# Kernel tuning notes

Measured on AMD Instinct MI355X. Metric: run time of the kernel, lower is better.

Reference implementation:

```python
import jax, jax.numpy as jnp
import numpy as np

N = 16384      # nodes
E = 262144     # edges (avg degree 16)
T = 4          # type_num
D = 64         # d_model
L = 2          # layers


def setup_inputs() -> dict:
    key = jax.random.key(0)
    ks = jax.random.split(key, 7)
    return {
        "x": jax.random.normal(ks[0], (N, D), dtype=jnp.float32),
        "edge_feature": jax.random.normal(ks[1], (T, D), dtype=jnp.float32),
        "theta": jax.random.normal(ks[2], (L, T, 3 * D), dtype=jnp.float32) * (1.0 / np.sqrt(3 * D)),
        "wr": jax.random.normal(ks[3], (L, D, D), dtype=jnp.float32) * (1.0 / np.sqrt(D)),
        "we": jax.random.normal(ks[4], (L, D, D), dtype=jnp.float32) * (1.0 / np.sqrt(D)),
        "edge_index": jax.random.randint(ks[5], (2, E), 0, N, dtype=jnp.int64),
        "edge_type": jax.random.randint(ks[6], (E,), 0, T, dtype=jnp.int64),
    }


def _scatter_softmax(r, row, num_nodes):
    # r: [T, E]; softmax over edges grouped by destination node `row`.
    rT = r.T  # [E, T] (segment ops reduce over leading axis)
    m = jax.ops.segment_max(rT, row, num_segments=num_nodes)   # [N, T]
    e = jnp.exp(rT - m[row])                                    # [E, T]
    s = jax.ops.segment_sum(e, row, num_segments=num_nodes)     # [N, T]
    return (e / s[row]).T                                       # [T, E]


def reference(x, edge_feature, theta, wr, we, edge_index, edge_type):
    n, d = x.shape
    t = edge_feature.shape[0]
    num_layers = theta.shape[0]
    row, col = edge_index[0], edge_index[1]

    h = jnp.broadcast_to(x[None], (t, n, d))  # x.expand(type_num, N, d)
    ef = edge_feature                          # [T, D]
    for i in range(num_layers):
        tg, thi, thj = theta[i, :, :d], theta[i, :, d:2 * d], theta[i, :, 2 * d:]
        # per-edge scores
        r_g = (tg @ ef.T)[:, edge_type]                        # [T, E]
        r_hi = jnp.einsum('tnd,td->tn', h, thi)[:, row]        # [T, E]
        r_hj = jnp.einsum('tnd,td->tn', h, thj)[:, col]        # [T, E]
        r = _scatter_softmax(r_g + r_hi + r_hj, row, n)        # [T, E]
        # gated messages
        ef = ef @ wr[i]                                        # [T, D]
        v_g = jax.nn.sigmoid(ef)[edge_type]                    # [E, D]
        v_h = jnp.einsum('tnd,de->tne', h, we[i])[:, col]      # [T, E, D]
        msg = r[:, :, None] * v_g[None] * v_h                  # [T, E, D]
        agg = jax.ops.segment_sum(jnp.moveaxis(msg, 1, 0), row, num_segments=n)  # [N, T, D]
        h = jnp.moveaxis(agg, 0, 1)                            # [T, N, D]
        if i < num_layers - 1:
            h = jax.nn.relu(h)      # dropout is identity in eval mode
            ef = jax.nn.relu(ef)
    return h
```

## Files before the change

kernel.cpp:

```cpp
#include <hip/hip_runtime.h>

#define NN 16384
#define EE 262144
#define TT 4
#define DD 64
#define SLOT 96
#define HB (EE / 256)
#define NB (NN / 64)

__device__ inline float g16_max(float v) {
    #pragma unroll
    for (int off = 1; off <= 8; off <<= 1) v = fmaxf(v, __shfl_xor(v, off));
    return v;
}
__device__ inline float g16_sum(float v) {
    #pragma unroll
    for (int off = 1; off <= 8; off <<= 1) v += __shfl_xor(v, off);
    return v;
}
__device__ inline float4 edge_group_reduce(float4 v) {
    #pragma unroll
    for (int off = 16; off < 64; off <<= 1) {
        v.x += __shfl_xor(v.x, off); v.y += __shfl_xor(v.y, off);
        v.z += __shfl_xor(v.z, off); v.w += __shfl_xor(v.w, off);
    }
    return v;
}
__device__ inline unsigned short f2bf(float f) {
    unsigned u = __float_as_uint(f);
    u += 0x7FFFu + ((u >> 16) & 1u);
    return (unsigned short)(u >> 16);
}
__device__ inline float bf2f(unsigned short h) {
    return __uint_as_float(((unsigned)h) << 16);
}
__device__ inline float4 bf4_to_f4(ushort4 h) {
    return float4{bf2f(h.x), bf2f(h.y), bf2f(h.z), bf2f(h.w)};
}

__global__ __launch_bounds__(256) void build_node0_kernel(
        const int* __restrict__ row, const int* __restrict__ col,
        const int* __restrict__ et, int* __restrict__ cnt,
        int* __restrict__ ce_slot,
        const float* __restrict__ x, const float* __restrict__ theta,
        const float* __restrict__ we, const float* __restrict__ ef_in,
        const float* __restrict__ wr,
        float* __restrict__ a, float* __restrict__ b,
        unsigned short* __restrict__ hw0,
        float* __restrict__ sg, float* __restrict__ rg) {
    __shared__ float h_lds[64][68];
    __shared__ float4 we_lds[64][16];
    __shared__ float th_lds[4][2][64];
    __shared__ float part_a[64][4][4];
    __shared__ float part_b[64][4][4];
    __shared__ float ef0[TT * DD];
    __shared__ float ef1[TT * DD];
    int tid = threadIdx.x;
    int bid = blockIdx.x;

    if (bid < HB) {
        int e = bid * 256 + tid;
        int r = row[e];
        int pos = atomicAdd(&cnt[r], 1);
        if (pos < SLOT)
            ce_slot[r * SLOT + pos] = col[e] | (et[e] << 14);
        return;
    }
    bid -= HB;

    if (bid == NB) {
        int t = tid >> 6, d = tid & 63;
        ef0[tid] = ef_in[tid];
        __syncthreads();
        if (tid < 16) {
            int tt = tid & 3, tq = tid >> 2;
            float s = 0.f;
            for (int k = 0; k < DD; ++k) s += theta[tq * 192 + k] * ef0[tt * DD + k];
            rg[tq * 4 + tt] = s;
        }
        float acc = 0.f;
        for (int k = 0; k < DD; ++k) acc += ef0[t * DD + k] * wr[k * DD + d];
        sg[tid] = 1.f / (1.f + __expf(-acc));
        ef1[tid] = fmaxf(acc, 0.f);
        __syncthreads();
        if (tid < 16) {
            int tt = tid & 3, tq = tid >> 2;
            float s = 0.f;
            for (int k = 0; k < DD; ++k) s += theta[(TT + tq) * 192 + k] * ef1[tt * DD + k];
            rg[16 + tq * 4 + tt] = s;
        }
        float acc2 = 0.f;
        for (int k = 0; k < DD; ++k) acc2 += ef1[t * DD + k] * wr[DD * DD + k * DD + d];
        sg[TT * DD + tid] = 1.f / (1.f + __expf(-acc2));
        return;
    }

    int n0 = bid * 64;
    {
        int q = tid & 15, nr = tid >> 4;
        #pragma unroll
        for (int r = 0; r < 4; ++r) {
            int n = r * 16 + nr;
            *(float4*)&h_lds[n][4 * q] = ((const float4*)x)[(n0 + n) * 16 + q];
        }
    }
    {
        const float4* we4 = (const float4*)we;
        #pragma unroll
        for (int r = 0; r < 4; ++r)
            ((float4*)we_lds)[tid + 256 * r] = we4[tid + 256 * r];
    }
    {
        #pragma unroll
        for (int r = 0; r < 2; ++r) {
            int e = tid + 256 * r;
            int t = e >> 7, ab = (e >> 6) & 1, k = e & 63;
            th_lds[t][ab][k] = theta[t * 192 + 64 + ab * 64 + k];
        }
    }
    __syncthreads();
    int i = tid >> 4, j = tid & 15;
    float4 acc[4];
    acc[0] = acc[1] = acc[2] = acc[3] = float4{0.f, 0.f, 0.f, 0.f};
    for (int k = 0; k < 64; ++k) {
        float4 wv = we_lds[k][j];
        #pragma unroll
        for (int r = 0; r < 4; ++r) {
            float hv = h_lds[4 * i + r][k];
            acc[r].x += hv * wv.x; acc[r].y += hv * wv.y;
            acc[r].z += hv * wv.z; acc[r].w += hv * wv.w;
        }
    }
    {
        int t = j >> 2, kq = j & 3;
        float pa[4] = {0, 0, 0, 0}, pb[4] = {0, 0, 0, 0};
        for (int kk = 0; kk < 16; ++kk) {
            int k = kq * 16 + kk;
            float ti = th_lds[t][0][k], tj = th_lds[t][1][k];
            #pragma unroll
            for (int r = 0; r < 4; ++r) {
                float hv = h_lds[4 * i + r][k];
                pa[r] += hv * ti; pb[r] += hv * tj;
            }
        }
        #pragma unroll
        for (int r = 0; r < 4; ++r) {
            part_a[4 * i + r][t][kq] = pa[r];
            part_b[4 * i + r][t][kq] = pb[r];
        }
    }
    #pragma unroll
    for (int r = 0; r < 4; ++r) {
        ushort4 hv;
        hv.x = f2bf(acc[r].x); hv.y = f2bf(acc[r].y);
        hv.z = f2bf(acc[r].z); hv.w = f2bf(acc[r].w);
        ((ushort4*)hw0)[(n0 + 4 * i + r) * 16 + j] = hv;
    }
    __syncthreads();
    {
        int n = tid >> 2, t = tid & 3;
        float4 va = *(float4*)&part_a[n][t][0];
        float4 vb = *(float4*)&part_b[n][t][0];
        a[t * NN + n0 + n] = va.x + va.y + va.z + va.w;
        b[t * NN + n0 + n] = vb.x + vb.y + vb.z + vb.w;
    }
}

__global__ __launch_bounds__(256) void node1_kernel(
        const float* __restrict__ h1, const float* __restrict__ theta,
        const float* __restrict__ we,
        float* __restrict__ a, float* __restrict__ b,
        unsigned short* __restrict__ hw) {
    __shared__ float h_lds[64][68];
    __shared__ float4 we_lds[64][16];
    __shared__ float th_lds[2][64];
    __shared__ float part_a[64][17];
    __shared__ float part_b[64][17];
    int tid = threadIdx.x;
    int t = blockIdx.y;
    int n0 = blockIdx.x * 64;
    const float* ht = h1 + (size_t)t * NN * DD;
    {
        int q = tid & 15, nr = tid >> 4;
        #pragma unroll
        for (int r = 0; r < 4; ++r) {
            int n = r * 16 + nr;
            *(float4*)&h_lds[n][4 * q] = ((const float4*)ht)[(n0 + n) * 16 + q];
        }
    }
    {
        const float4* we4 = (const float4*)(we + DD * DD);
        #pragma unroll
        for (int r = 0; r < 4; ++r)
            ((float4*)we_lds)[tid + 256 * r] = we4[tid + 256 * r];
    }
    if (tid < 128) {
        int ab = tid >> 6, k = tid & 63;
        th_lds[ab][k] = theta[(TT + t) * 192 + 64 + ab * 64 + k];
    }
    __syncthreads();
    int i = tid >> 4, j = tid & 15;
    float4 acc[4];
    acc[0] = acc[1] = acc[2] = acc[3] = float4{0.f, 0.f, 0.f, 0.f};
    for (int k = 0; k < 64; ++k) {
        float4 wv = we_lds[k][j];
        #pragma unroll
        for (int r = 0; r < 4; ++r) {
            float hv = h_lds[4 * i + r][k];
            acc[r].x += hv * wv.x; acc[r].y += hv * wv.y;
            acc[r].z += hv * wv.z; acc[r].w += hv * wv.w;
        }
    }
    {
        float pa[4] = {0, 0, 0, 0}, pb[4] = {0, 0, 0, 0};
        #pragma unroll
        for (int kk = 0; kk < 4; ++kk) {
            int k = 4 * j + kk;
            float ti = th_lds[0][k], tj = th_lds[1][k];
            #pragma unroll
            for (int r = 0; r < 4; ++r) {
                float hv = h_lds[4 * i + r][k];
                pa[r] += hv * ti; pb[r] += hv * tj;
            }
        }
        #pragma unroll
        for (int r = 0; r < 4; ++r) {
            part_a[4 * i + r][j] = pa[r];
            part_b[4 * i + r][j] = pb[r];
        }
    }
    #pragma unroll
    for (int r = 0; r < 4; ++r) {
        ushort4 hv;
        hv.x = f2bf(acc[r].x); hv.y = f2bf(acc[r].y);
        hv.z = f2bf(acc[r].z); hv.w = f2bf(acc[r].w);
        ((ushort4*)hw)[((size_t)t * NN + n0 + 4 * i + r) * 16 + j] = hv;
    }
    __syncthreads();
    if (tid < 64) {
        float s = 0.f;
        #pragma unroll
        for (int jj = 0; jj < 16; ++jj) s += part_a[tid][jj];
        a[t * NN + n0 + tid] = s;
    } else if (tid < 128) {
        int n = tid - 64;
        float s = 0.f;
        #pragma unroll
        for (int jj = 0; jj < 16; ++jj) s += part_b[n][jj];
        b[t * NN + n0 + n] = s;
    }
}

__global__ __launch_bounds__(256) void edge_agg0_kernel(
        const int* __restrict__ cnt, const int* __restrict__ ce_slot,
        const float* __restrict__ a, const float* __restrict__ b,
        const float* __restrict__ rg, const float* __restrict__ sg,
        const unsigned short* __restrict__ hw0, float* __restrict__ h1) {
    __shared__ float4 sg4[TT * 16];
    __shared__ float rg_lds[16];
    __shared__ int cols[4][SLOT];
    __shared__ float wT[4][SLOT][4];
    int tid = threadIdx.x;
    if (tid < 64) sg4[tid] = ((const float4*)sg)[tid];
    if (tid < 16) rg_lds[tid] = rg[tid];
    int w = tid >> 6, lane = tid & 63;
    int n = blockIdx.x * 4 + w;
    int deg = cnt[n];
    if (deg > SLOT) deg = SLOT;
    const int* ces = ce_slot + n * SLOT;
    int tl = lane >> 4, il = lane & 15;
    __syncthreads();

    float a_n = a[tl * NN + n];
    const float* bt = b + tl * NN;
    float m_l = -INFINITY, s_l = 0.f;
    for (int e = il; e < deg; e += 16) {
        int pk = ces[e];
        int c = pk & 16383, tt = pk >> 14;
        float rp = a_n + bt[c] + rg_lds[tl * 4 + tt];
        wT[w][e][tl] = rp;
        if (tl == 0) cols[w][e] = pk;
        if (rp > m_l) { s_l = s_l * __expf(m_l - rp) + 1.f; m_l = rp; }
        else          { s_l += __expf(rp - m_l); }
    }
    float m = g16_max(m_l);
    float s = g16_sum((m_l > -INFINITY) ? s_l * __expf(m_l - m) : 0.f);
    float inv_s = (s > 0.f) ? 1.f / s : 0.f;
    for (int e = il; e < deg; e += 16)
        wT[w][e][tl] = __expf(wT[w][e][tl] - m) * inv_s;
    __syncthreads();

    int eg = lane >> 4, q = lane & 15;
    float4 acc0{0,0,0,0}, acc1{0,0,0,0}, acc2{0,0,0,0}, acc3{0,0,0,0};
    const ushort4* hw4 = (const ushort4*)hw0;
    for (int base = 0; base < deg; base += 4) {
        int e = base + eg;
        if (e < deg) {
            int pk = cols[w][e];
            int c = pk & 16383, tt = pk >> 14;
            ushort4 hv = hw4[c * 16 + q];
            float4 sgv = sg4[tt * 16 + q];
            float4 wv = *(float4*)&wT[w][e][0];
            float4 f = bf4_to_f4(hv);
            float4 g{sgv.x * f.x, sgv.y * f.y, sgv.z * f.z, sgv.w * f.w};
            acc0.x += wv.x * g.x; acc0.y += wv.x * g.y; acc0.z += wv.x * g.z; acc0.w += wv.x * g.w;
            acc1.x += wv.y * g.x; acc1.y += wv.y * g.y; acc1.z += wv.y * g.z; acc1.w += wv.y * g.w;
            acc2.x += wv.z * g.x; acc2.y += wv.z * g.y; acc2.z += wv.z * g.z; acc2.w += wv.z * g.w;
            acc3.x += wv.w * g.x; acc3.y += wv.w * g.y; acc3.z += wv.w * g.z; acc3.w += wv.w * g.w;
        }
    }
    acc0 = edge_group_reduce(acc0);
    acc1 = edge_group_reduce(acc1);
    acc2 = edge_group_reduce(acc2);
    acc3 = edge_group_reduce(acc3);
    float4 o = acc0;
    if (eg == 1) o = acc1;
    if (eg == 2) o = acc2;
    if (eg == 3) o = acc3;
    o.x = fmaxf(o.x, 0.f); o.y = fmaxf(o.y, 0.f);
    o.z = fmaxf(o.z, 0.f); o.w = fmaxf(o.w, 0.f);
    ((float4*)h1)[(eg * NN + n) * 16 + q] = o;
}

__global__ __launch_bounds__(256) void edge_agg1_kernel(
        const int* __restrict__ cnt, const int* __restrict__ ce_slot,
        const float* __restrict__ a, const float* __restrict__ b,
        const float* __restrict__ rg, const float* __restrict__ sg,
        const unsigned short* __restrict__ hw, float* __restrict__ out) {
    __shared__ float4 sg4[TT * 16];
    __shared__ float rg_lds[16];
    __shared__ int cols[4][SLOT];
    __shared__ float wT[4][SLOT][4];
    int tid = threadIdx.x;
    if (tid < 64) sg4[tid] = ((const float4*)sg)[tid];
    if (tid < 16) rg_lds[tid] = rg[tid];
    int w = tid >> 6, lane = tid & 63;
    int n = blockIdx.x * 4 + w;
    int deg = cnt[n];
    if (deg > SLOT) deg = SLOT;
    const int* ces = ce_slot + n * SLOT;
    int tl = lane >> 4, il = lane & 15;
    __syncthreads();

    float a_n = a[tl * NN + n];
    const float* bt = b + tl * NN;
    float m_l = -INFINITY, s_l = 0.f;
    for (int e = il; e < deg; e += 16) {
        int pk = ces[e];
        int c = pk & 16383, tt = pk >> 14;
        float rp = a_n + bt[c] + rg_lds[tl * 4 + tt];
        wT[w][e][tl] = rp;
        if (tl == 0) cols[w][e] = pk;
        if (rp > m_l) { s_l = s_l * __expf(m_l - rp) + 1.f; m_l = rp; }
        else          { s_l += __expf(rp - m_l); }
    }
    float m = g16_max(m_l);
    float s = g16_sum((m_l > -INFINITY) ? s_l * __expf(m_l - m) : 0.f);
    float inv_s = (s > 0.f) ? 1.f / s : 0.f;
    for (int e = il; e < deg; e += 16)
        wT[w][e][tl] = __expf(wT[w][e][tl] - m) * inv_s;
    __syncthreads();

    int eg = lane >> 4, q = lane & 15;
    float4 acc0{0,0,0,0}, acc1{0,0,0,0}, acc2{0,0,0,0}, acc3{0,0,0,0};
    const ushort4* hw4 = (const ushort4*)hw;
    for (int base = 0; base < deg; base += 4) {
        int e = base + eg;
        if (e < deg) {
            int pk = cols[w][e];
            int c = pk & 16383, tt = pk >> 14;
            int ba = c * 16 + q;
            ushort4 h0 = hw4[ba];
            ushort4 h1v = hw4[NN * 16 + ba];
            ushort4 h2 = hw4[2 * NN * 16 + ba];
            ushort4 h3 = hw4[3 * NN * 16 + ba];
            float4 sgv = sg4[tt * 16 + q];
            float4 wv = *(float4*)&wT[w][e][0];
            float4 f0 = bf4_to_f4(h0), f1 = bf4_to_f4(h1v);
            float4 f2 = bf4_to_f4(h2), f3 = bf4_to_f4(h3);
            acc0.x += wv.x * sgv.x * f0.x; acc0.y += wv.x * sgv.y * f0.y;
            acc0.z += wv.x * sgv.z * f0.z; acc0.w += wv.x * sgv.w * f0.w;
            acc1.x += wv.y * sgv.x * f1.x; acc1.y += wv.y * sgv.y * f1.y;
            acc1.z += wv.y * sgv.z * f1.z; acc1.w += wv.y * sgv.w * f1.w;
            acc2.x += wv.z * sgv.x * f2.x; acc2.y += wv.z * sgv.y * f2.y;
            acc2.z += wv.z * sgv.z * f2.z; acc2.w += wv.z * sgv.w * f2.w;
            acc3.x += wv.w * sgv.x * f3.x; acc3.y += wv.w * sgv.y * f3.y;
            acc3.z += wv.w * sgv.z * f3.z; acc3.w += wv.w * sgv.w * f3.w;
        }
    }
    acc0 = edge_group_reduce(acc0);
    acc1 = edge_group_reduce(acc1);
    acc2 = edge_group_reduce(acc2);
    acc3 = edge_group_reduce(acc3);
    float4 o = acc0;
    if (eg == 1) o = acc1;
    if (eg == 2) o = acc2;
    if (eg == 3) o = acc3;
    ((float4*)out)[(eg * NN + n) * 16 + q] = o;
}

extern "C" void kernel_launch(void* const* d_in, const int* in_sizes, int n_in,
                              void* d_out, int out_size, void* d_ws, size_t ws_size,
                              hipStream_t stream) {
    const float* x     = (const float*)d_in[0];
    const float* ef_in = (const float*)d_in[1];
    const float* theta = (const float*)d_in[2];
    const float* wr    = (const float*)d_in[3];
    const float* we    = (const float*)d_in[4];
    const int* edge_index = (const int*)d_in[5];
    const int* edge_type  = (const int*)d_in[6];
    float* out = (float*)d_out;

    const int* row = edge_index;
    const int* col = edge_index + EE;

    char* p = (char*)d_ws;
    auto alloc = [&](size_t bytes) { void* r = (void*)p; p += (bytes + 255) & ~(size_t)255; return r; };
    int*   cnt     = (int*)  alloc((size_t)NN * 4);
    int*   ce_slot = (int*)  alloc((size_t)NN * SLOT * 4);
    float* a       = (float*)alloc((size_t)TT * NN * 4);
    float* b       = (float*)alloc((size_t)TT * NN * 4);
    unsigned short* hw0 = (unsigned short*)alloc((size_t)NN * DD * 2);
    unsigned short* hw  = (unsigned short*)alloc((size_t)TT * NN * DD * 2);
    float* h1      = (float*)alloc((size_t)TT * NN * DD * 4);
    float* sg      = (float*)alloc((size_t)2 * TT * DD * 4);
    float* rg      = (float*)alloc((size_t)2 * 16 * 4);

    hipMemsetAsync(cnt, 0, (size_t)NN * 4, stream);
    build_node0_kernel<<<HB + NB + 1, 256, 0, stream>>>(
        row, col, edge_type, cnt, ce_slot, x, theta, we, ef_in, wr,
        a, b, hw0, sg, rg);
    edge_agg0_kernel<<<NN / 4, 256, 0, stream>>>(cnt, ce_slot, a, b, rg, sg, hw0, h1);
    node1_kernel<<<dim3(NN / 64, TT), 256, 0, stream>>>(h1, theta, we, a, b, hw);
    edge_agg1_kernel<<<NN / 4, 256, 0, stream>>>(cnt, ce_slot, a, b,
                                                 rg + 16, sg + TT * DD, hw, out);
}
```

Measured before the change: 146.8 us.

## Fuse layer-1 node transform into edge aggregation and interleave score arrays

Removes the separate node1 kernel: edge_agg0 now keeps the relu'd layer-0 output for its 4 nodes in shared memory and directly computes the we[1] projection, the bf16 hw1 and the a/b attention scores. This avoids writing and re-reading the fp32 h1 tensor (16 MB) and drops one launch. The a/b scores move to a node-major [N,4] layout so each edge fetches all four types with one float4 load. The softmax now runs one edge per lane across the full wave with four online accumulators. The fused matmul reads we from global/L1 per k instead of LDS and uses only 16 rows per block, so reuse is lower.

```diff
diff --git a/kernel.cpp b/kernel.cpp
--- a/kernel.cpp
+++ b/kernel.cpp
@@ -8,14 +8,14 @@
 #define HB (EE / 256)
 #define NB (NN / 64)
 
-__device__ inline float g16_max(float v) {
-    #pragma unroll
-    for (int off = 1; off <= 8; off <<= 1) v = fmaxf(v, __shfl_xor(v, off));
+__device__ inline float wave_reduce_max(float v) {
+    #pragma unroll
+    for (int off = 32; off >= 1; off >>= 1) v = fmaxf(v, __shfl_xor(v, off));
     return v;
 }
-__device__ inline float g16_sum(float v) {
-    #pragma unroll
-    for (int off = 1; off <= 8; off <<= 1) v += __shfl_xor(v, off);
+__device__ inline float wave_reduce_sum(float v) {
+    #pragma unroll
+    for (int off = 32; off >= 1; off >>= 1) v += __shfl_xor(v, off);
     return v;
 }
 __device__ inline float4 edge_group_reduce(float4 v) {
@@ -37,6 +37,9 @@
 __device__ inline float4 bf4_to_f4(ushort4 h) {
     return float4{bf2f(h.x), bf2f(h.y), bf2f(h.z), bf2f(h.w)};
 }
+
+#define ONL(mm, ss, r) { if ((r) > (mm)) { ss = ss * __expf(mm - (r)) + 1.f; mm = (r); } \
+                         else ss += __expf((r) - (mm)); }
 
 __global__ __launch_bounds__(256) void build_node0_kernel(
         const int* __restrict__ row, const int* __restrict__ col,
@@ -45,7 +48,7 @@
         const float* __restrict__ x, const float* __restrict__ theta,
         const float* __restrict__ we, const float* __restrict__ ef_in,
         const float* __restrict__ wr,
-        float* __restrict__ a, float* __restrict__ b,
+        float* __restrict__ a4, float* __restrict__ b4,
         unsigned short* __restrict__ hw0,
         float* __restrict__ sg, float* __restrict__ rg) {
     __shared__ float h_lds[64][68];
@@ -161,134 +164,69 @@
         int n = tid >> 2, t = tid & 3;
         float4 va = *(float4*)&part_a[n][t][0];
         float4 vb = *(float4*)&part_b[n][t][0];
-        a[t * NN + n0 + n] = va.x + va.y + va.z + va.w;
-        b[t * NN + n0 + n] = vb.x + vb.y + vb.z + vb.w;
-    }
-}
-
-__global__ __launch_bounds__(256) void node1_kernel(
-        const float* __restrict__ h1, const float* __restrict__ theta,
-        const float* __restrict__ we,
-        float* __restrict__ a, float* __restrict__ b,
-        unsigned short* __restrict__ hw) {
-    __shared__ float h_lds[64][68];
-    __shared__ float4 we_lds[64][16];
-    __shared__ float th_lds[2][64];
-    __shared__ float part_a[64][17];
-    __shared__ float part_b[64][17];
-    int tid = threadIdx.x;
-    int t = blockIdx.y;
-    int n0 = blockIdx.x * 64;
-    const float* ht = h1 + (size_t)t * NN * DD;
-    {
-        int q = tid & 15, nr = tid >> 4;
-        #pragma unroll
-        for (int r = 0; r < 4; ++r) {
-            int n = r * 16 + nr;
-            *(float4*)&h_lds[n][4 * q] = ((const float4*)ht)[(n0 + n) * 16 + q];
-        }
-    }
-    {
-        const float4* we4 = (const float4*)(we + DD * DD);
-        #pragma unroll
-        for (int r = 0; r < 4; ++r)
-            ((float4*)we_lds)[tid + 256 * r] = we4[tid + 256 * r];
-    }
-    if (tid < 128) {
-        int ab = tid >> 6, k = tid & 63;
-        th_lds[ab][k] = theta[(TT + t) * 192 + 64 + ab * 64 + k];
-    }
-    __syncthreads();
-    int i = tid >> 4, j = tid & 15;
-    float4 acc[4];
-    acc[0] = acc[1] = acc[2] = acc[3] = float4{0.f, 0.f, 0.f, 0.f};
-    for (int k = 0; k < 64; ++k) {
-        float4 wv = we_lds[k][j];
-        #pragma unroll
-        for (int r = 0; r < 4; ++r) {
-            float hv = h_lds[4 * i + r][k];
-            acc[r].x += hv * wv.x; acc[r].y += hv * wv.y;
-            acc[r].z += hv * wv.z; acc[r].w += hv * wv.w;
-        }
-    }
-    {
-        float pa[4] = {0, 0, 0, 0}, pb[4] = {0, 0, 0, 0};
-        #pragma unroll
-        for (int kk = 0; kk < 4; ++kk) {
-            int k = 4 * j + kk;
-            float ti = th_lds[0][k], tj = th_lds[1][k];
-            #pragma unroll
-            for (int r = 0; r < 4; ++r) {
-                float hv = h_lds[4 * i + r][k];
-                pa[r] += hv * ti; pb[r] += hv * tj;
-            }
-        }
-        #pragma unroll
-        for (int r = 0; r < 4; ++r) {
-            part_a[4 * i + r][j] = pa[r];
-            part_b[4 * i + r][j] = pb[r];
-        }
-    }
-    #pragma unroll
-    for (int r = 0; r < 4; ++r) {
-        ushort4 hv;
-        hv.x = f2bf(acc[r].x); hv.y = f2bf(acc[r].y);
-        hv.z = f2bf(acc[r].z); hv.w = f2bf(acc[r].w);
-        ((ushort4*)hw)[((size_t)t * NN + n0 + 4 * i + r) * 16 + j] = hv;
-    }
-    __syncthreads();
-    if (tid < 64) {
-        float s = 0.f;
-        #pragma unroll
-        for (int jj = 0; jj < 16; ++jj) s += part_a[tid][jj];
-        a[t * NN + n0 + tid] = s;
-    } else if (tid < 128) {
-        int n = tid - 64;
-        float s = 0.f;
-        #pragma unroll
-        for (int jj = 0; jj < 16; ++jj) s += part_b[n][jj];
-        b[t * NN + n0 + n] = s;
+        a4[(n0 + n) * 4 + t] = va.x + va.y + va.z + va.w;
+        b4[(n0 + n) * 4 + t] = vb.x + vb.y + vb.z + vb.w;
     }
 }
 
 __global__ __launch_bounds__(256) void edge_agg0_kernel(
         const int* __restrict__ cnt, const int* __restrict__ ce_slot,
-        const float* __restrict__ a, const float* __restrict__ b,
+        const float* __restrict__ a4, const float* __restrict__ b4,
         const float* __restrict__ rg, const float* __restrict__ sg,
-        const unsigned short* __restrict__ hw0, float* __restrict__ h1) {
-    __shared__ float4 sg4[TT * 16];
-    __shared__ float rg_lds[16];
+        const unsigned short* __restrict__ hw0,
+        const float* __restrict__ we, const float* __restrict__ theta,
+        float* __restrict__ a4o, float* __restrict__ b4o,
+        unsigned short* __restrict__ hw1) {
+    __shared__ float4 sg4[64];
+    __shared__ float4 rg4[4];
     __shared__ int cols[4][SLOT];
-    __shared__ float wT[4][SLOT][4];
+    __shared__ float4 wT[4][SLOT];
+    __shared__ float h1_lds[16][68];
+    __shared__ float th1[4][2][64];
+    __shared__ float part_a[16][17];
+    __shared__ float part_b[16][17];
     int tid = threadIdx.x;
     if (tid < 64) sg4[tid] = ((const float4*)sg)[tid];
-    if (tid < 16) rg_lds[tid] = rg[tid];
+    if (tid < 4)  rg4[tid] = float4{rg[tid], rg[4 + tid], rg[8 + tid], rg[12 + tid]};
+    #pragma unroll
+    for (int r2 = 0; r2 < 2; ++r2) {
+        int e2 = tid + 256 * r2;
+        int t2 = e2 >> 7, ab = (e2 >> 6) & 1, k = e2 & 63;
+        th1[t2][ab][k] = theta[(TT + t2) * 192 + 64 + ab * 64 + k];
+    }
     int w = tid >> 6, lane = tid & 63;
     int n = blockIdx.x * 4 + w;
-    int deg = cnt[n];
-    if (deg > SLOT) deg = SLOT;
+    int deg = cnt[n]; if (deg > SLOT) deg = SLOT;
     const int* ces = ce_slot + n * SLOT;
-    int tl = lane >> 4, il = lane & 15;
-    __syncthreads();
-
-    float a_n = a[tl * NN + n];
-    const float* bt = b + tl * NN;
-    float m_l = -INFINITY, s_l = 0.f;
-    for (int e = il; e < deg; e += 16) {
+    float4 av = ((const float4*)a4)[n];
+    __syncthreads();
+
+    float m0 = -INFINITY, m1 = -INFINITY, m2 = -INFINITY, m3 = -INFINITY;
+    float s0 = 0.f, s1 = 0.f, s2 = 0.f, s3 = 0.f;
+    for (int e = lane; e < deg; e += 64) {
         int pk = ces[e];
         int c = pk & 16383, tt = pk >> 14;
-        float rp = a_n + bt[c] + rg_lds[tl * 4 + tt];
-        wT[w][e][tl] = rp;
-        if (tl == 0) cols[w][e] = pk;
-        if (rp > m_l) { s_l = s_l * __expf(m_l - rp) + 1.f; m_l = rp; }
-        else          { s_l += __expf(rp - m_l); }
-    }
-    float m = g16_max(m_l);
-    float s = g16_sum((m_l > -INFINITY) ? s_l * __expf(m_l - m) : 0.f);
-    float inv_s = (s > 0.f) ? 1.f / s : 0.f;
-    for (int e = il; e < deg; e += 16)
-        wT[w][e][tl] = __expf(wT[w][e][tl] - m) * inv_s;
-    __syncthreads();
+        float4 bv = ((const float4*)b4)[c];
+        float4 rv = rg4[tt];
+        float4 rp{av.x + bv.x + rv.x, av.y + bv.y + rv.y,
+                  av.z + bv.z + rv.z, av.w + bv.w + rv.w};
+        cols[w][e] = pk;
+        wT[w][e] = rp;
+        ONL(m0, s0, rp.x) ONL(m1, s1, rp.y) ONL(m2, s2, rp.z) ONL(m3, s3, rp.w)
+    }
+    float M0 = wave_reduce_max(m0), M1 = wave_reduce_max(m1);
+    float M2 = wave_reduce_max(m2), M3 = wave_reduce_max(m3);
+    float S0 = wave_reduce_sum((m0 > -INFINITY) ? s0 * __expf(m0 - M0) : 0.f);
+    float S1 = wave_reduce_sum((m1 > -INFINITY) ? s1 * __expf(m1 - M1) : 0.f);
+    float S2 = wave_reduce_sum((m2 > -INFINITY) ? s2 * __expf(m2 - M2) : 0.f);
+    float S3 = wave_reduce_sum((m3 > -INFINITY) ? s3 * __expf(m3 - M3) : 0.f);
+    float i0 = (S0 > 0.f) ? 1.f / S0 : 0.f, i1 = (S1 > 0.f) ? 1.f / S1 : 0.f;
+    float i2 = (S2 > 0.f) ? 1.f / S2 : 0.f, i3 = (S3 > 0.f) ? 1.f / S3 : 0.f;
+    for (int e = lane; e < deg; e += 64) {
+        float4 rp = wT[w][e];
+        wT[w][e] = float4{__expf(rp.x - M0) * i0, __expf(rp.y - M1) * i1,
+                          __expf(rp.z - M2) * i2, __expf(rp.w - M3) * i3};
+    }
 
     int eg = lane >> 4, q = lane & 15;
     float4 acc0{0,0,0,0}, acc1{0,0,0,0}, acc2{0,0,0,0}, acc3{0,0,0,0};
@@ -300,7 +238,7 @@
             int c = pk & 16383, tt = pk >> 14;
             ushort4 hv = hw4[c * 16 + q];
             float4 sgv = sg4[tt * 16 + q];
-            float4 wv = *(float4*)&wT[w][e][0];
+            float4 wv = wT[w][e];
             float4 f = bf4_to_f4(hv);
             float4 g{sgv.x * f.x, sgv.y * f.y, sgv.z * f.z, sgv.w * f.w};
             acc0.x += wv.x * g.x; acc0.y += wv.x * g.y; acc0.z += wv.x * g.z; acc0.w += wv.x * g.w;
@@ -319,47 +257,91 @@
     if (eg == 3) o = acc3;
     o.x = fmaxf(o.x, 0.f); o.y = fmaxf(o.y, 0.f);
     o.z = fmaxf(o.z, 0.f); o.w = fmaxf(o.w, 0.f);
-    ((float4*)h1)[(eg * NN + n) * 16 + q] = o;
+    *(float4*)&h1_lds[eg * 4 + w][4 * q] = o;
+    __syncthreads();
+
+    int r = tid >> 4, j = tid & 15;
+    int t1 = r >> 2, wn = r & 3;
+    int n1 = blockIdx.x * 4 + wn;
+    const float4* we2 = (const float4*)(we + DD * DD);
+    float4 ga{0,0,0,0};
+    for (int k = 0; k < 64; ++k) {
+        float hv = h1_lds[r][k];
+        float4 wv = we2[k * 16 + j];
+        ga.x += hv * wv.x; ga.y += hv * wv.y;
+        ga.z += hv * wv.z; ga.w += hv * wv.w;
+    }
+    float pa = 0.f, pb = 0.f;
+    #pragma unroll
+    for (int kk = 0; kk < 4; ++kk) {
+        int k = 4 * j + kk;
+        float hv = h1_lds[r][k];
+        pa += hv * th1[t1][0][k]; pb += hv * th1[t1][1][k];
+    }
+    part_a[r][j] = pa; part_b[r][j] = pb;
+    ushort4 hb;
+    hb.x = f2bf(ga.x); hb.y = f2bf(ga.y); hb.z = f2bf(ga.z); hb.w = f2bf(ga.w);
+    ((ushort4*)hw1)[((size_t)t1 * NN + n1) * 16 + j] = hb;
+    __syncthreads();
+    if (tid < 16) {
+        float s = 0.f;
+        #pragma unroll
+        for (int jj = 0; jj < 16; ++jj) s += part_a[tid][jj];
+        a4o[(blockIdx.x * 4 + (tid & 3)) * 4 + (tid >> 2)] = s;
+    } else if (tid < 32) {
+        int r3 = tid - 16;
+        float s = 0.f;
+        #pragma unroll
+        for (int jj = 0; jj < 16; ++jj) s += part_b[r3][jj];
+        b4o[(blockIdx.x * 4 + (r3 & 3)) * 4 + (r3 >> 2)] = s;
+    }
 }
 
 __global__ __launch_bounds__(256) void edge_agg1_kernel(
         const int* __restrict__ cnt, const int* __restrict__ ce_slot,
-        const float* __restrict__ a, const float* __restrict__ b,
+        const float* __restrict__ a4, const float* __restrict__ b4,
         const float* __restrict__ rg, const float* __restrict__ sg,
         const unsigned short* __restrict__ hw, float* __restrict__ out) {
-    __shared__ float4 sg4[TT * 16];
-    __shared__ float rg_lds[16];
+    __shared__ float4 sg4[64];
+    __shared__ float4 rg4[4];
     __shared__ int cols[4][SLOT];
-    __shared__ float wT[4][SLOT][4];
+    __shared__ float4 wT[4][SLOT];
     int tid = threadIdx.x;
     if (tid < 64) sg4[tid] = ((const float4*)sg)[tid];
-    if (tid < 16) rg_lds[tid] = rg[tid];
+    if (tid < 4)  rg4[tid] = float4{rg[tid], rg[4 + tid], rg[8 + tid], rg[12 + tid]};
     int w = tid >> 6, lane = tid & 63;
     int n = blockIdx.x * 4 + w;
-    int deg = cnt[n];
-    if (deg > SLOT) deg = SLOT;
+    int deg = cnt[n]; if (deg > SLOT) deg = SLOT;
     const int* ces = ce_slot + n * SLOT;
-    int tl = lane >> 4, il = lane & 15;
-    __syncthreads();
-
-    float a_n = a[tl * NN + n];
-    const float* bt = b + tl * NN;
-    float m_l = -INFINITY, s_l = 0.f;
-    for (int e = il; e < deg; e += 16) {
+    float4 av = ((const float4*)a4)[n];
+    __syncthreads();
+
+    float m0 = -INFINITY, m1 = -INFINITY, m2 = -INFINITY, m3 = -INFINITY;
+    float s0 = 0.f, s1 = 0.f, s2 = 0.f, s3 = 0.f;
+    for (int e = lane; e < deg; e += 64) {
         int pk = ces[e];
         int c = pk & 16383, tt = pk >> 14;
-        float rp = a_n + bt[c] + rg_lds[tl * 4 + tt];
-        wT[w][e][tl] = rp;
-        if (tl == 0) cols[w][e] = pk;
-        if (rp > m_l) { s_l = s_l * __expf(m_l - rp) + 1.f; m_l = rp; }
-        else          { s_l += __expf(rp - m_l); }
-    }
-    float m = g16_max(m_l);
-    float s = g16_sum((m_l > -INFINITY) ? s_l * __expf(m_l - m) : 0.f);
-    float inv_s = (s > 0.f) ? 1.f / s : 0.f;
-    for (int e = il; e < deg; e += 16)
-        wT[w][e][tl] = __expf(wT[w][e][tl] - m) * inv_s;
-    __syncthreads();
+        float4 bv = ((const float4*)b4)[c];
+        float4 rv = rg4[tt];
+        float4 rp{av.x + bv.x + rv.x, av.y + bv.y + rv.y,
+                  av.z + bv.z + rv.z, av.w + bv.w + rv.w};
+        cols[w][e] = pk;
+        wT[w][e] = rp;
+        ONL(m0, s0, rp.x) ONL(m1, s1, rp.y) ONL(m2, s2, rp.z) ONL(m3, s3, rp.w)
+    }
+    float M0 = wave_reduce_max(m0), M1 = wave_reduce_max(m1);
+    float M2 = wave_reduce_max(m2), M3 = wave_reduce_max(m3);
+    float S0 = wave_reduce_sum((m0 > -INFINITY) ? s0 * __expf(m0 - M0) : 0.f);
+    float S1 = wave_reduce_sum((m1 > -INFINITY) ? s1 * __expf(m1 - M1) : 0.f);
+    float S2 = wave_reduce_sum((m2 > -INFINITY) ? s2 * __expf(m2 - M2) : 0.f);
+    float S3 = wave_reduce_sum((m3 > -INFINITY) ? s3 * __expf(m3 - M3) : 0.f);
+    float i0 = (S0 > 0.f) ? 1.f / S0 : 0.f, i1 = (S1 > 0.f) ? 1.f / S1 : 0.f;
+    float i2 = (S2 > 0.f) ? 1.f / S2 : 0.f, i3 = (S3 > 0.f) ? 1.f / S3 : 0.f;
+    for (int e = lane; e < deg; e += 64) {
+        float4 rp = wT[w][e];
+        wT[w][e] = float4{__expf(rp.x - M0) * i0, __expf(rp.y - M1) * i1,
+                          __expf(rp.z - M2) * i2, __expf(rp.w - M3) * i3};
+    }
 
     int eg = lane >> 4, q = lane & 15;
     float4 acc0{0,0,0,0}, acc1{0,0,0,0}, acc2{0,0,0,0}, acc3{0,0,0,0};
@@ -375,7 +357,7 @@
             ushort4 h2 = hw4[2 * NN * 16 + ba];
             ushort4 h3 = hw4[3 * NN * 16 + ba];
             float4 sgv = sg4[tt * 16 + q];
-            float4 wv = *(float4*)&wT[w][e][0];
+            float4 wv = wT[w][e];
             float4 f0 = bf4_to_f4(h0), f1 = bf4_to_f4(h1v);
             float4 f2 = bf4_to_f4(h2), f3 = bf4_to_f4(h3);
             acc0.x += wv.x * sgv.x * f0.x; acc0.y += wv.x * sgv.y * f0.y;
@@ -418,20 +400,21 @@
     auto alloc = [&](size_t bytes) { void* r = (void*)p; p += (bytes + 255) & ~(size_t)255; return r; };
     int*   cnt     = (int*)  alloc((size_t)NN * 4);
     int*   ce_slot = (int*)  alloc((size_t)NN * SLOT * 4);
-    float* a       = (float*)alloc((size_t)TT * NN * 4);
-    float* b       = (float*)alloc((size_t)TT * NN * 4);
+    float* a4_0    = (float*)alloc((size_t)NN * 4 * 4);
+    float* b4_0    = (float*)alloc((size_t)NN * 4 * 4);
+    float* a4_1    = (float*)alloc((size_t)NN * 4 * 4);
+    float* b4_1    = (float*)alloc((size_t)NN * 4 * 4);
     unsigned short* hw0 = (unsigned short*)alloc((size_t)NN * DD * 2);
-    unsigned short* hw  = (unsigned short*)alloc((size_t)TT * NN * DD * 2);
-    float* h1      = (float*)alloc((size_t)TT * NN * DD * 4);
+    unsigned short* hw1 = (unsigned short*)alloc((size_t)TT * NN * DD * 2);
     float* sg      = (float*)alloc((size_t)2 * TT * DD * 4);
     float* rg      = (float*)alloc((size_t)2 * 16 * 4);
 
     hipMemsetAsync(cnt, 0, (size_t)NN * 4, stream);
     build_node0_kernel<<<HB + NB + 1, 256, 0, stream>>>(
         row, col, edge_type, cnt, ce_slot, x, theta, we, ef_in, wr,
-        a, b, hw0, sg, rg);
-    edge_agg0_kernel<<<NN / 4, 256, 0, stream>>>(cnt, ce_slot, a, b, rg, sg, hw0, h1);
-    node1_kernel<<<dim3(NN / 64, TT), 256, 0, stream>>>(h1, theta, we, a, b, hw);
-    edge_agg1_kernel<<<NN / 4, 256, 0, stream>>>(cnt, ce_slot, a, b,
-                                                 rg + 16, sg + TT * DD, hw, out);
-}
+        a4_0, b4_0, hw0, sg, rg);
+    edge_agg0_kernel<<<NN / 4, 256, 0, stream>>>(
+        cnt, ce_slot, a4_0, b4_0, rg, sg, hw0, we, theta, a4_1, b4_1, hw1);
+    edge_agg1_kernel<<<NN / 4, 256, 0, stream>>>(
+        cnt, ce_slot, a4_1, b4_1, rg + 16, sg + TT * DD, hw1, out);
+}
```

New measurement: 156.8 us. 6.8% more time.
